# Optimization experiments

Measured on AMD Instinct MI355X. Metric: run time of the kernel, lower is better.

## Reference

```python
import jax, jax.numpy as jnp
import numpy as np

B, T, N = 512, 200, 256
ENC_G, ENC_C = 256, 256
C_DIM, G_DIM, U_DIM, F_DIM = 128, 256, 64, 64
CLIP = 5.0


def _gru(x, h, Wih, Whh, bih, bhh):
    # PyTorch nn.GRUCell math
    gi = x @ Wih.T + bih
    gh = h @ Whh.T + bhh
    ir, iz, inn = jnp.split(gi, 3, axis=-1)
    hr, hz, hn = jnp.split(gh, 3, axis=-1)
    r = jax.nn.sigmoid(ir + hr)
    z = jax.nn.sigmoid(iz + hz)
    n = jnp.tanh(inn + r * hn)
    return (1.0 - z) * n + z * h


def setup_inputs() -> dict:
    key = jax.random.key(0)
    ks = iter(jax.random.split(key, 64))

    def gru_p(i, h):
        return (jax.random.normal(next(ks), (3 * h, i)) * i ** -0.5,
                jax.random.normal(next(ks), (3 * h, h)) * h ** -0.5,
                jnp.zeros(3 * h), jnp.zeros(3 * h))

    def lin_p(i, o):
        return (jax.random.normal(next(ks), (o, i)) * i ** -0.5, jnp.zeros(o))

    inp = {}
    inp['x'] = jax.random.uniform(next(ks), (B, T, N))
    inp['eps_g0'] = jax.random.normal(next(ks), (B, G_DIM))
    inp['eps_u'] = jax.random.normal(next(ks), (B, T, U_DIM))
    for name, (i, h) in [('gf', (N, ENC_G)), ('gb', (N, ENC_G)),
                         ('cf', (N, ENC_C)), ('cb', (N, ENC_C)),
                         ('ct', (2 * ENC_C + F_DIM, C_DIM)), ('gn', (U_DIM, G_DIM))]:
        Wih, Whh, bih, bhh = gru_p(i, h)
        inp['Wih_' + name] = Wih; inp['Whh_' + name] = Whh
        inp['bih_' + name] = bih; inp['bhh_' + name] = bhh
    for name, (i, o) in [('g0m', (2 * ENC_G, G_DIM)), ('g0v', (2 * ENC_G, G_DIM)),
                         ('um', (C_DIM, U_DIM)), ('uv', (C_DIM, U_DIM)),
                         ('f', (G_DIM, F_DIM)), ('r', (F_DIM, N))]:
        W, b = lin_p(i, o)
        inp['W_' + name] = W; inp['b_' + name] = b
    return inp


def reference(x, eps_g0, eps_u,
              Wih_gf, Whh_gf, bih_gf, bhh_gf,
              Wih_gb, Whh_gb, bih_gb, bhh_gb,
              Wih_cf, Whh_cf, bih_cf, bhh_cf,
              Wih_cb, Whh_cb, bih_cb, bhh_cb,
              Wih_ct, Whh_ct, bih_ct, bhh_ct,
              Wih_gn, Whh_gn, bih_gn, bhh_gn,
              W_g0m, b_g0m, W_g0v, b_g0v,
              W_um, b_um, W_uv, b_uv,
              W_f, b_f, W_r, b_r):
    Bsz = x.shape[0]
    xs = x.transpose(1, 0, 2)  # [T, B, N]
    zg = jnp.zeros((Bsz, ENC_G), x.dtype)
    zc = jnp.zeros((Bsz, ENC_C), x.dtype)

    def make_enc(pg, pc):
        def step(carry, xt):
            hg, hc = carry
            hg = jnp.minimum(_gru(xt, hg, *pg), CLIP)   # clamp(max=clip_val)
            hc = jnp.minimum(_gru(xt, hc, *pc), CLIP)
            return (hg, hc), hc
        return step

    (hgf, _), hcf = jax.lax.scan(
        make_enc((Wih_gf, Whh_gf, bih_gf, bhh_gf), (Wih_cf, Whh_cf, bih_cf, bhh_cf)),
        (zg, zc), xs)
    (hgb, _), hcb = jax.lax.scan(
        make_enc((Wih_gb, Whh_gb, bih_gb, bhh_gb), (Wih_cb, Whh_cb, bih_cb, bhh_cb)),
        (zg, zc), xs[::-1])
    h_enc_g = jnp.concatenate([hgf, hgb], axis=-1)        # [B, 2*ENC_G]
    h_enc_c = jnp.concatenate([hcf, hcb[::-1]], axis=-1)  # [T, B, 2*ENC_C]

    g0_mean = h_enc_g @ W_g0m.T + b_g0m
    g0_logv = jnp.log(jnp.exp(h_enc_g @ W_g0v.T + b_g0v) + 1e-4)
    g0 = eps_g0 * jnp.exp(0.5 * g0_logv) + g0_mean

    f0 = g0 @ W_f.T + b_f
    hc0 = jnp.zeros((Bsz, C_DIM), x.dtype)

    def gen_step(carry, inp):
        h_c, g, f = carry
        henc_t, eps_t = inp
        cin = jnp.concatenate([henc_t, f], axis=-1)
        h_c = jnp.clip(_gru(cin, h_c, Wih_ct, Whh_ct, bih_ct, bhh_ct), 0.0, CLIP)
        um = h_c @ W_um.T + b_um
        ul = h_c @ W_uv.T + b_uv
        u = eps_t * jnp.exp(0.5 * ul) + um
        g = jnp.clip(_gru(u, g, Wih_gn, Whh_gn, bih_gn, bhh_gn), 0.0, CLIP)
        f = g @ W_f.T + b_f
        return (h_c, g, f), (um, ul, f)

    _, (u_means, u_logvs, factors) = jax.lax.scan(
        gen_step, (hc0, g0, f0), (h_enc_c, eps_u.transpose(1, 0, 2)))
    factors = factors.transpose(1, 0, 2)  # [B, T, F_DIM]
    rates = jnp.exp(jnp.clip(factors @ W_r.T + b_r, -CLIP, CLIP))
    return (g0_mean, g0_logv,
            u_means.transpose(1, 0, 2), u_logvs.transpose(1, 0, 2),
            factors, rates)
```

## Files before the change

kernel.cpp:

```cpp
#include <hip/hip_runtime.h>
#include <hip/hip_bf16.h>
#include <stdint.h>

typedef __bf16 bf16x8 __attribute__((ext_vector_type(8)));
typedef __bf16 bf16x4 __attribute__((ext_vector_type(4)));
typedef float  f32x4  __attribute__((ext_vector_type(4)));
typedef unsigned short u16x8 __attribute__((ext_vector_type(8)));

#define MFMA_B16(A_,B_,C_) __builtin_amdgcn_mfma_f32_16x16x32_bf16((A_),(B_),(C_),0,0,0)

static constexpr int TT = 200;
static constexpr int TC = 25;
static constexpr int NCH = 8;

static __device__ __forceinline__ float sig_f(float x){ return 1.f/(1.f+__expf(-x)); }
static __device__ __forceinline__ float tanh_f(float x){
  float e = __expf(-2.f*fabsf(x));
  float t = (1.f-e)/(1.f+e);
  return x<0.f ? -t : t;
}
static __device__ __forceinline__ float bf2f(unsigned short u){
  union{unsigned int i; float f;} v; v.i = ((unsigned)u)<<16; return v.f;
}
static __device__ __forceinline__ void pin8(bf16x8 &v){ asm volatile("" : "+v"(v)); }

static __device__ __forceinline__ int swz_off(int row, int col_bytes, int strideB){
  return (row*strideB + col_bytes) ^ ((row&7)<<4);
}
static __device__ __forceinline__ bf16x8 lds_rdA(const __bf16* buf, int row, int kt, int lq, int strideB){
  return *(const bf16x8*)((const char*)buf + swz_off(row, kt*64 + lq*16, strideB));
}
static __device__ __forceinline__ void lds_wr(__bf16* buf, int row, int dim, int strideB, float v){
  *(__bf16*)((char*)buf + swz_off(row, dim*2, strideB)) = (__bf16)v;
}
static __device__ __forceinline__ void lds_barrier(){
  asm volatile("s_waitcnt lgkmcnt(0)" ::: "memory");
  __builtin_amdgcn_s_barrier();
}

__global__ void cvt_bf16(const float* __restrict__ s, __bf16* __restrict__ d, int n){
  int i = blockIdx.x*blockDim.x + threadIdx.x;
  int st = gridDim.x*blockDim.x;
  for(; i<n; i+=st) d[i] = (__bf16)s[i];
}

__global__ __launch_bounds__(256) void gi_gemm(const float* __restrict__ x,
                                               const __bf16* __restrict__ Wall,
                                               __bf16* __restrict__ gi, int t0){
  const int tid=threadIdx.x, w=tid>>6, l=tid&63, lr=l&15, lq=l>>4;
  const int cell = blockIdx.y;
  const bool fwd = (cell&1)==0;
  const int m0 = blockIdx.x*64;
  const int tloc = m0>>9, b0 = m0&511;
  const int tabs = fwd ? (t0+tloc) : (TT-1-(t0+tloc));
  const int brow = b0 + w*16 + lr;

  const float* xp = x + (size_t)brow*TT*256 + (size_t)tabs*256 + lq*8;
  bf16x8 a[8];
  #pragma unroll
  for(int kt=0;kt<8;kt++){
    float4 f0 = *(const float4*)(xp + kt*32);
    float4 f1 = *(const float4*)(xp + kt*32 + 4);
    bf16x8 v;
    v[0]=(__bf16)f0.x; v[1]=(__bf16)f0.y; v[2]=(__bf16)f0.z; v[3]=(__bf16)f0.w;
    v[4]=(__bf16)f1.x; v[5]=(__bf16)f1.y; v[6]=(__bf16)f1.z; v[7]=(__bf16)f1.w;
    a[kt]=v;
  }
  const __bf16* Wc = Wall + (size_t)cell*768*256;
  #pragma unroll 1
  for(int nt=0;nt<48;nt++){
    f32x4 acc={};
    const __bf16* bp = Wc + (size_t)(nt*16+lr)*256 + lq*8;
    #pragma unroll
    for(int kt=0;kt<8;kt++)
      acc = MFMA_B16(a[kt], *(const bf16x8*)(bp + kt*32), acc);
    bf16x4 pk;
    pk[0]=(__bf16)acc[0]; pk[1]=(__bf16)acc[1]; pk[2]=(__bf16)acc[2]; pk[3]=(__bf16)acc[3];
    *(bf16x4*)(gi + (((size_t)cell*TC + tloc)*768 + nt*16+lr)*512 + b0 + w*16 + lq*4) = pk;
  }
}

struct EncP{
  const __bf16* whh;
  const float*  bih[4];
  const float*  bhh[4];
  const __bf16* gi;
  __bf16* henc;
  float*  hcar;
  int t0;
};
__global__ __launch_bounds__(512,2) void enc_scan(EncP P){
  const int tid=threadIdx.x, w=tid>>6, l=tid&63, lr=l&15, lq=l>>4;
  const int cell=blockIdx.y, b0=blockIdx.x*16;
  const bool fwd = (cell&1)==0;
  const bool isC = cell>=2;
  const int dim0 = w*32;

  __shared__ __align__(16) __bf16 hA[2][16*256];
  __shared__ __align__(16) __bf16 giL[2][768*16];
  __shared__ float blds[1024];

  for(int d=tid; d<256; d+=512){
    blds[d]     = P.bih[cell][d]     + P.bhh[cell][d];
    blds[256+d] = P.bih[cell][256+d] + P.bhh[cell][256+d];
    blds[512+d] = P.bih[cell][512+d];
    blds[768+d] = P.bhh[cell][512+d];
  }
  const __bf16* Wh = P.whh + (size_t)cell*768*256;
  bf16x8 wreg[2][2][8];
  #pragma unroll
  for(int jt=0;jt<2;jt++)
    #pragma unroll
    for(int g=0;g<2;g++)
      #pragma unroll
      for(int kt=0;kt<8;kt++){
        wreg[jt][g][kt] = *(const bf16x8*)(Wh + (size_t)(g*256 + dim0 + jt*16 + lr)*256 + kt*32 + lq*8);
        pin8(wreg[jt][g][kt]);
      }
  f32x4 hold[2];
  #pragma unroll
  for(int jt=0;jt<2;jt++)
    #pragma unroll
    for(int rr=0;rr<4;rr++){
      float v = P.hcar[((size_t)cell*512 + b0 + lq*4+rr)*256 + dim0 + jt*16 + lr];
      hold[jt][rr] = v;
      lds_wr(hA[0], lq*4+rr, dim0+jt*16+lr, 512, v);
    }
  const int prow = w*96 + (l>>1), phal = l&1;
  const __bf16* gbase = P.gi + ((size_t)cell*TC*768 + prow)*512 + b0 + phal*8;
  u16x8 pf0, pf1, pf2;
  pf0 = *(const u16x8*)(gbase + (size_t)0*768*512 +  0*512);
  pf1 = *(const u16x8*)(gbase + (size_t)0*768*512 + 32*512);
  pf2 = *(const u16x8*)(gbase + (size_t)0*768*512 + 64*512);
  __syncthreads();
  {
    __bf16* gl = giL[0] + prow*16 + phal*8;
    *(u16x8*)(gl)        = pf0;
    *(u16x8*)(gl+32*16)  = pf1;
    *(u16x8*)(gl+64*16)  = pf2;
  }
  { int sn = 1 < TC ? 1 : TC-1;
    pf0 = *(const u16x8*)(gbase + (size_t)sn*768*512 +  0*512);
    pf1 = *(const u16x8*)(gbase + (size_t)sn*768*512 + 32*512);
    pf2 = *(const u16x8*)(gbase + (size_t)sn*768*512 + 64*512);
  }
  lds_barrier();

  int p=0, q=0;
  #pragma unroll 1
  for(int s=0;s<TC;s++){
    const int tglob = P.t0 + s;
    const int tx = fwd ? tglob : (TT-1-tglob);
    if(s+1<TC){
      __bf16* gl = giL[1-q] + prow*16 + phal*8;
      *(u16x8*)(gl)        = pf0;
      *(u16x8*)(gl+32*16)  = pf1;
      *(u16x8*)(gl+64*16)  = pf2;
    }
    { int sn = (s+2<TC) ? s+2 : TC-1;
      pf0 = *(const u16x8*)(gbase + (size_t)sn*768*512 +  0*512);
      pf1 = *(const u16x8*)(gbase + (size_t)sn*768*512 + 32*512);
      pf2 = *(const u16x8*)(gbase + (size_t)sn*768*512 + 64*512);
    }
    const __bf16* gq = giL[q];
    #pragma unroll
    for(int jt=0;jt<2;jt++){
      const int d = dim0 + jt*16 + lr;
      const __bf16* whN = Wh + (size_t)(512 + d)*256 + lq*8;
      f32x4 aR={}, aZ={}, aH={};
      #pragma unroll
      for(int kt=0;kt<8;kt++){
        bf16x8 frag = lds_rdA(hA[p], lr, kt, lq, 512);
        aR = MFMA_B16(frag, wreg[jt][0][kt], aR);
        aZ = MFMA_B16(frag, wreg[jt][1][kt], aZ);
        aH = MFMA_B16(frag, *(const bf16x8*)(whN + kt*32), aH);
      }
      ushort4 gR = *(const ushort4*)(gq + (0*256+d)*16 + lq*4);
      ushort4 gZ = *(const ushort4*)(gq + (1*256+d)*16 + lq*4);
      ushort4 gN = *(const ushort4*)(gq + (2*256+d)*16 + lq*4);
      const float bR=blds[d], bZ=blds[256+d], bI=blds[512+d], bH=blds[768+d];
      const unsigned short* uR=(const unsigned short*)&gR;
      const unsigned short* uZ=(const unsigned short*)&gZ;
      const unsigned short* uN=(const unsigned short*)&gN;
      #pragma unroll
      for(int rr=0;rr<4;rr++){
        float r = sig_f(aR[rr] + bf2f(uR[rr]) + bR);
        float z = sig_f(aZ[rr] + bf2f(uZ[rr]) + bZ);
        float nn= tanh_f(bf2f(uN[rr]) + bI + r*(aH[rr] + bH));
        float h = (1.f-z)*nn + z*hold[jt][rr];
        h = fminf(h, 5.f);
        hold[jt][rr] = h;
        lds_wr(hA[1-p], lq*4+rr, d, 512, h);
      }
    }
    if(isC){
      const int row = l>>2, dgrp = (l&3)*8;
      bf16x8 hv = *(const bf16x8*)((const char*)hA[1-p] +
                    ((row*512 + (dim0+dgrp)*2) ^ ((row&7)<<4)));
      *(bf16x8*)(P.henc + ((size_t)tx*512 + b0 + row)*512 + (cell==3?256:0) + dim0 + dgrp) = hv;
    }
    lds_barrier();
    p ^= 1; q ^= 1;
  }
  #pragma unroll
  for(int jt=0;jt<2;jt++)
    #pragma unroll
    for(int rr=0;rr<4;rr++)
      P.hcar[((size_t)cell*512 + b0 + lq*4+rr)*256 + dim0 + jt*16 + lr] = hold[jt][rr];
}

__global__ void g0_kernel(const float* __restrict__ hgf, const float* __restrict__ hgb,
                          const float* __restrict__ Wm, const float* __restrict__ bm,
                          const float* __restrict__ Wv, const float* __restrict__ bv,
                          const float* __restrict__ eps,
                          float* __restrict__ o_mean, float* __restrict__ o_logv,
                          float* __restrict__ g0){
  int j = blockIdx.x*blockDim.x + threadIdx.x;
  int b = j>>8, d = j&255;
  const float4* hf=(const float4*)(hgf + (size_t)b*256);
  const float4* hb=(const float4*)(hgb + (size_t)b*256);
  const float4* mp=(const float4*)(Wm + (size_t)d*512);
  const float4* vp=(const float4*)(Wv + (size_t)d*512);
  float am=0.f, av=0.f;
  #pragma unroll 4
  for(int k=0;k<64;k++){
    float4 h=hf[k], m=mp[k], v=vp[k];
    am += h.x*m.x + h.y*m.y + h.z*m.z + h.w*m.w;
    av += h.x*v.x + h.y*v.y + h.z*v.z + h.w*v.w;
  }
  #pragma unroll 4
  for(int k=0;k<64;k++){
    float4 h=hb[k], m=mp[64+k], v=vp[64+k];
    am += h.x*m.x + h.y*m.y + h.z*m.z + h.w*m.w;
    av += h.x*v.x + h.y*v.y + h.z*v.z + h.w*v.w;
  }
  float mean = am + bm[d];
  float ev   = __expf(av + bv[d]) + 1e-4f;
  float lv   = __logf(ev);
  o_mean[j]=mean; o_logv[j]=lv;
  g0[j] = eps[j]*sqrtf(ev) + mean;
}

__global__ __launch_bounds__(256,2) void gict_gemm(const __bf16* __restrict__ henc,
                                                   const __bf16* __restrict__ wct,
                                                   __bf16* __restrict__ gictT){
  const int tid=threadIdx.x, w=tid>>6, l=tid&63, lr=l&15, lq=l>>4;
  const int m0 = blockIdx.x*8 + w*2;
  bf16x8 a[2][16];
  #pragma unroll
  for(int m=0;m<2;m++){
    const __bf16* ap = henc + (size_t)((m0+m)*16 + lr)*512 + lq*8;
    #pragma unroll
    for(int kt=0;kt<16;kt++) a[m][kt] = *(const bf16x8*)(ap + kt*32);
  }
  #pragma unroll 1
  for(int nt=0;nt<24;nt++){
    f32x4 c0={}, c1={};
    const __bf16* bp = wct + (size_t)(nt*16+lr)*576 + lq*8;
    #pragma unroll
    for(int kt=0;kt<16;kt++){
      bf16x8 bb = *(const bf16x8*)(bp + kt*32);
      c0 = MFMA_B16(a[0][kt], bb, c0);
      c1 = MFMA_B16(a[1][kt], bb, c1);
    }
    #pragma unroll
    for(int m=0;m<2;m++){
      f32x4 c = m? c1 : c0;
      int R0 = (m0+m)*16 + lq*4;
      int t  = R0>>9, b = R0&511;
      bf16x4 pk;
      pk[0]=(__bf16)c[0]; pk[1]=(__bf16)c[1]; pk[2]=(__bf16)c[2]; pk[3]=(__bf16)c[3];
      *(bf16x4*)(gictT + ((size_t)t*384 + nt*16+lr)*512 + b) = pk;
    }
  }
}

struct GenP{
  const __bf16 *wct, *whh_ct, *wih_gn, *whh_gn, *w_um, *w_uv, *w_f;
  const float  *bih_ct, *bhh_ct, *bih_gn, *bhh_gn, *b_um, *b_uv, *b_f;
  const __bf16* gihT;
  const float*  g0;
  const float*  eps_u;
  float *o_um, *o_ul, *o_f;
};
__global__ __launch_bounds__(512,2) void gen_scan(GenP P){
  const int tid=threadIdx.x, w=tid>>6, l=tid&63, lr=l&15, lq=l>>4;
  const int b0 = blockIdx.x*16;

  __shared__ __align__(16) __bf16 wgnL[768*64];
  __shared__ __align__(16) __bf16 hcA[2][16*128];
  __shared__ __align__(16) __bf16 gA [2][16*256];
  __shared__ __align__(16) __bf16 uA [16*64];
  __shared__ __align__(16) __bf16 fA [16*64];

  for(int c=tid; c<6144; c+=512){
    int row = c>>3, part = c&7;
    bf16x8 v = *(const bf16x8*)(P.wih_gn + (size_t)row*64 + part*8);
    *(bf16x8*)((char*)wgnL + ((row*128 + part*16) ^ ((row&7)<<4))) = v;
  }
  bf16x8 wrz[2][2][8];
  #pragma unroll
  for(int jt=0;jt<2;jt++)
    #pragma unroll
    for(int g=0;g<2;g++)
      #pragma unroll
      for(int kt=0;kt<8;kt++){
        wrz[jt][g][kt] = *(const bf16x8*)(P.whh_gn + (size_t)(g*256 + w*32 + jt*16 + lr)*256 + kt*32 + lq*8);
        pin8(wrz[jt][g][kt]);
      }

  const int dct = w*16 + lr;
  const int duu = (w&3)*16 + lr;
  const int duf = (w&3)*16 + lr;
  const float bctR = P.bih_ct[dct]     + P.bhh_ct[dct];
  const float bctZ = P.bih_ct[128+dct] + P.bhh_ct[128+dct];
  const float bctI = P.bih_ct[256+dct];
  const float bctH = P.bhh_ct[256+dct];
  float bgnR[2], bgnZ[2], bgnI[2], bgnH[2];
  #pragma unroll
  for(int jt=0;jt<2;jt++){
    int d = w*32 + jt*16 + lr;
    bgnR[jt] = P.bih_gn[d]     + P.bhh_gn[d];
    bgnZ[jt] = P.bih_gn[256+d] + P.bhh_gn[256+d];
    bgnI[jt] = P.bih_gn[512+d];
    bgnH[jt] = P.bhh_gn[512+d];
  }
  const float bum = P.b_um[duu], buv = P.b_uv[duu], bff = P.b_f[duf];

  f32x4 gC[2], hcC;
  hcC = (f32x4){};
  #pragma unroll
  for(int jt=0;jt<2;jt++)
    #pragma unroll
    for(int rr=0;rr<4;rr++){
      float v = P.g0[(size_t)(b0+lq*4+rr)*256 + w*32 + jt*16 + lr];
      gC[jt][rr] = v;
      lds_wr(gA[0], lq*4+rr, w*32+jt*16+lr, 512, v);
    }
  for(int i=tid;i<16*128;i+=512) hcA[0][i] = (__bf16)0.f;
  __syncthreads();
  if(w>=4){
    f32x4 fa={};
    #pragma unroll
    for(int kt=0;kt<8;kt++){
      bf16x8 gf = lds_rdA(gA[0], lr, kt, lq, 512);
      fa = MFMA_B16(gf, *(const bf16x8*)(P.w_f + (size_t)duf*256 + kt*32 + lq*8), fa);
    }
    #pragma unroll
    for(int rr=0;rr<4;rr++) lds_wr(fA, lq*4+rr, duf, 128, fa[rr]+bff);
  }
  ushort4 gpR, gpZ, gpN; float epf[4];
  gpR = *(const ushort4*)(P.gihT + ((size_t)0*384 +       dct)*512 + b0 + lq*4);
  gpZ = *(const ushort4*)(P.gihT + ((size_t)0*384 + 128 + dct)*512 + b0 + lq*4);
  gpN = *(const ushort4*)(P.gihT + ((size_t)0*384 + 256 + dct)*512 + b0 + lq*4);
  if(w<4){
    #pragma unroll
    for(int rr=0;rr<4;rr++) epf[rr] = P.eps_u[((size_t)(b0+lq*4+rr)*TT + 0)*64 + duu];
  }
  bf16x8 cwh[3][4];
  #pragma unroll
  for(int g=0;g<3;g++)
    #pragma unroll
    for(int kt=0;kt<4;kt++)
      cwh[g][kt] = *(const bf16x8*)(P.whh_ct + (size_t)(g*128+dct)*128 + kt*32 + lq*8);
  __syncthreads();

  int pc=0, pg=0;
  #pragma unroll 1
  for(int t=0;t<TT;t++){
    {
      bf16x8 ff0 = lds_rdA(fA, lr, 0, lq, 128);
      bf16x8 ff1 = lds_rdA(fA, lr, 1, lq, 128);
      bf16x8 hp0 = lds_rdA(hcA[pc], lr, 0, lq, 256);
      bf16x8 hp1 = lds_rdA(hcA[pc], lr, 1, lq, 256);
      bf16x8 hp2 = lds_rdA(hcA[pc], lr, 2, lq, 256);
      bf16x8 hp3 = lds_rdA(hcA[pc], lr, 3, lq, 256);
      f32x4 aR={}, aZ={}, aI={}, aH={};
      #pragma unroll
      for(int g=0;g<3;g++){
        const __bf16* wif = P.wct + (size_t)(g*128+dct)*576 + 512 + lq*8;
        bf16x8 wf0 = *(const bf16x8*)(wif);
        bf16x8 wf1 = *(const bf16x8*)(wif + 32);
        if(g==0){
          aR = MFMA_B16(ff0,wf0,aR); aR = MFMA_B16(ff1,wf1,aR);
          aR = MFMA_B16(hp0,cwh[0][0],aR); aR = MFMA_B16(hp1,cwh[0][1],aR);
          aR = MFMA_B16(hp2,cwh[0][2],aR); aR = MFMA_B16(hp3,cwh[0][3],aR);
        }else if(g==1){
          aZ = MFMA_B16(ff0,wf0,aZ); aZ = MFMA_B16(ff1,wf1,aZ);
          aZ = MFMA_B16(hp0,cwh[1][0],aZ); aZ = MFMA_B16(hp1,cwh[1][1],aZ);
          aZ = MFMA_B16(hp2,cwh[1][2],aZ); aZ = MFMA_B16(hp3,cwh[1][3],aZ);
        }else{
          aI = MFMA_B16(ff0,wf0,aI); aI = MFMA_B16(ff1,wf1,aI);
          aH = MFMA_B16(hp0,cwh[2][0],aH); aH = MFMA_B16(hp1,cwh[2][1],aH);
          aH = MFMA_B16(hp2,cwh[2][2],aH); aH = MFMA_B16(hp3,cwh[2][3],aH);
        }
      }
      const unsigned short* uR=(const unsigned short*)&gpR;
      const unsigned short* uZ=(const unsigned short*)&gpZ;
      const unsigned short* uN=(const unsigned short*)&gpN;
      #pragma unroll
      for(int rr=0;rr<4;rr++){
        float r = sig_f(aR[rr] + bf2f(uR[rr]) + bctR);
        float z = sig_f(aZ[rr] + bf2f(uZ[rr]) + bctZ);
        float nn= tanh_f(aI[rr] + bf2f(uN[rr]) + bctI + r*(aH[rr] + bctH));
        float h = (1.f-z)*nn + z*hcC[rr];
        h = fminf(fmaxf(h,0.f), 5.f);
        hcC[rr] = h;
        lds_wr(hcA[1-pc], lq*4+rr, dct, 256, h);
      }
    }
    lds_barrier();

    if(w<4){
      bf16x8 hn0 = lds_rdA(hcA[1-pc], lr, 0, lq, 256);
      bf16x8 hn1 = lds_rdA(hcA[1-pc], lr, 1, lq, 256);
      bf16x8 hn2 = lds_rdA(hcA[1-pc], lr, 2, lq, 256);
      bf16x8 hn3 = lds_rdA(hcA[1-pc], lr, 3, lq, 256);
      f32x4 am={}, av={};
      const __bf16* wm = P.w_um + (size_t)duu*128 + lq*8;
      const __bf16* wv = P.w_uv + (size_t)duu*128 + lq*8;
      am = MFMA_B16(hn0, *(const bf16x8*)(wm   ), am);
      am = MFMA_B16(hn1, *(const bf16x8*)(wm+32), am);
      am = MFMA_B16(hn2, *(const bf16x8*)(wm+64), am);
      am = MFMA_B16(hn3, *(const bf16x8*)(wm+96), am);
      av = MFMA_B16(hn0, *(const bf16x8*)(wv   ), av);
      av = MFMA_B16(hn1, *(const bf16x8*)(wv+32), av);
      av = MFMA_B16(hn2, *(const bf16x8*)(wv+64), av);
      av = MFMA_B16(hn3, *(const bf16x8*)(wv+96), av);
      #pragma unroll
      for(int rr=0;rr<4;rr++){
        const int row = lq*4+rr;
        float um = am[rr] + bum;
        float ul = av[rr] + buv;
        size_t oi = ((size_t)(b0+row)*TT + t)*64 + duu;
        P.o_um[oi] = um;
        P.o_ul[oi] = ul;
        float u = epf[rr]*__expf(0.5f*ul) + um;
        lds_wr(uA, row, duu, 128, u);
      }
    }
    bf16x8 wn0[8];
    #pragma unroll
    for(int kt=0;kt<8;kt++)
      wn0[kt] = *(const bf16x8*)(P.whh_gn + (size_t)(512 + w*32 + lr)*256 + kt*32 + lq*8);
    lds_barrier();

    {
      const int tn = (t+1<TT)? t+1 : TT-1;
      gpR = *(const ushort4*)(P.gihT + ((size_t)tn*384 +       dct)*512 + b0 + lq*4);
      gpZ = *(const ushort4*)(P.gihT + ((size_t)tn*384 + 128 + dct)*512 + b0 + lq*4);
      gpN = *(const ushort4*)(P.gihT + ((size_t)tn*384 + 256 + dct)*512 + b0 + lq*4);
      if(w<4){
        #pragma unroll
        for(int rr=0;rr<4;rr++) epf[rr] = P.eps_u[((size_t)(b0+lq*4+rr)*TT + tn)*64 + duu];
      }
      bf16x8 uf0 = lds_rdA(uA, lr, 0, lq, 128);
      bf16x8 uf1 = lds_rdA(uA, lr, 1, lq, 128);
      #pragma unroll
      for(int jt=0;jt<2;jt++){
        const int dg = w*32 + jt*16 + lr;
        bf16x8 wn[8];
        if(jt==0){
          #pragma unroll
          for(int kt=0;kt<8;kt++) wn[kt] = wn0[kt];
        }else{
          #pragma unroll
          for(int kt=0;kt<8;kt++)
            wn[kt] = *(const bf16x8*)(P.whh_gn + (size_t)(512 + dg)*256 + kt*32 + lq*8);
        }
        f32x4 aR={}, aZ={}, aI={}, aH={};
        #pragma unroll
        for(int g=0;g<3;g++){
          const int row = g*256 + dg;
          bf16x8 w0 = *(const bf16x8*)((const char*)wgnL + ((row*128 +  0 + lq*16) ^ ((row&7)<<4)));
          bf16x8 w1 = *(const bf16x8*)((const char*)wgnL + ((row*128 + 64 + lq*16) ^ ((row&7)<<4)));
          if(g==0){ aR = MFMA_B16(uf0,w0,aR); aR = MFMA_B16(uf1,w1,aR); }
          else if(g==1){ aZ = MFMA_B16(uf0,w0,aZ); aZ = MFMA_B16(uf1,w1,aZ); }
          else { aI = MFMA_B16(uf0,w0,aI); aI = MFMA_B16(uf1,w1,aI); }
        }
        #pragma unroll
        for(int kt=0;kt<8;kt++){
          bf16x8 gf = lds_rdA(gA[pg], lr, kt, lq, 512);
          aR = MFMA_B16(gf, wrz[jt][0][kt], aR);
          aZ = MFMA_B16(gf, wrz[jt][1][kt], aZ);
          aH = MFMA_B16(gf, wn[kt], aH);
        }
        #pragma unroll
        for(int rr=0;rr<4;rr++){
          float r = sig_f(aR[rr] + bgnR[jt]);
          float z = sig_f(aZ[rr] + bgnZ[jt]);
          float nn= tanh_f(aI[rr] + bgnI[jt] + r*(aH[rr] + bgnH[jt]));
          float gv = (1.f-z)*nn + z*gC[jt][rr];
          gv = fminf(fmaxf(gv,0.f), 5.f);
          gC[jt][rr] = gv;
          lds_wr(gA[1-pg], lq*4+rr, dg, 512, gv);
        }
      }
    }
    lds_barrier();

    if(w>=4){
      f32x4 fa={};
      const __bf16* wfp = P.w_f + (size_t)duf*256 + lq*8;
      #pragma unroll
      for(int kt=0;kt<8;kt++){
        bf16x8 gf = lds_rdA(gA[1-pg], lr, kt, lq, 512);
        fa = MFMA_B16(gf, *(const bf16x8*)(wfp + kt*32), fa);
      }
      #pragma unroll
      for(int rr=0;rr<4;rr++){
        const int row = lq*4+rr;
        float v = fa[rr] + bff;
        P.o_f[((size_t)(b0+row)*TT + t)*64 + duf] = v;
        lds_wr(fA, row, duf, 128, v);
      }
    }
    #pragma unroll
    for(int g=0;g<3;g++)
      #pragma unroll
      for(int kt=0;kt<4;kt++)
        cwh[g][kt] = *(const bf16x8*)(P.whh_ct + (size_t)(g*128+dct)*128 + kt*32 + lq*8);
    lds_barrier();
    pc ^= 1; pg ^= 1;
  }
}

__global__ void rates_k(const float* __restrict__ fac, const float* __restrict__ Wr,
                        const float* __restrict__ br, float* __restrict__ out){
  const int total = 512*200*256;
  int i = blockIdx.x*blockDim.x + threadIdx.x;
  int st = gridDim.x*blockDim.x;
  for(; i<total; i+=st){
    int row = i>>8, n = i&255;
    const float4* fp=(const float4*)(fac + (size_t)row*64);
    const float4* wp=(const float4*)(Wr  + (size_t)n*64);
    float a = 0.f;
    #pragma unroll
    for(int k=0;k<16;k++){
      float4 f=fp[k], ww=wp[k];
      a += f.x*ww.x + f.y*ww.y + f.z*ww.z + f.w*ww.w;
    }
    a += br[n];
    a = fminf(fmaxf(a, -5.f), 5.f);
    out[i] = __expf(a);
  }
}

extern "C" void kernel_launch(void* const* d_in, const int* in_sizes, int n_in,
                              void* d_out, int out_size, void* d_ws, size_t ws_size,
                              hipStream_t stream){
  (void)in_sizes; (void)n_in; (void)out_size; (void)ws_size;
  const float* x      = (const float*)d_in[0];
  const float* eps_g0 = (const float*)d_in[1];
  const float* eps_u  = (const float*)d_in[2];
  const float* Wih_f[6]; const float* Whh_f[6]; const float* bih[6]; const float* bhh[6];
  for(int c=0;c<6;c++){
    Wih_f[c]=(const float*)d_in[3+4*c]; Whh_f[c]=(const float*)d_in[4+4*c];
    bih[c]  =(const float*)d_in[5+4*c]; bhh[c]  =(const float*)d_in[6+4*c];
  }
  const float* W_g0m=(const float*)d_in[27]; const float* b_g0m=(const float*)d_in[28];
  const float* W_g0v=(const float*)d_in[29]; const float* b_g0v=(const float*)d_in[30];
  const float* W_um =(const float*)d_in[31]; const float* b_um =(const float*)d_in[32];
  const float* W_uv =(const float*)d_in[33]; const float* b_uv =(const float*)d_in[34];
  const float* W_f  =(const float*)d_in[35]; const float* b_f  =(const float*)d_in[36];
  const float* W_r  =(const float*)d_in[37]; const float* b_r  =(const float*)d_in[38];

  char* ws = (char*)d_ws; size_t off = 0;
  auto alloc = [&](size_t bytes)->char*{
    char* p = ws + off; off = (off + bytes + 255) & ~(size_t)255; return p;
  };
  __bf16* wencall = (__bf16*)alloc((size_t)4*768*256*2);
  __bf16* whhall  = (__bf16*)alloc((size_t)4*768*256*2);
  __bf16* wct_b   = (__bf16*)alloc((size_t)384*576*2);
  __bf16* whhct_b = (__bf16*)alloc((size_t)384*128*2);
  __bf16* wihgn_b = (__bf16*)alloc((size_t)768*64*2);
  __bf16* whhgn_b = (__bf16*)alloc((size_t)768*256*2);
  __bf16* wum_b   = (__bf16*)alloc((size_t)64*128*2);
  __bf16* wuv_b   = (__bf16*)alloc((size_t)64*128*2);
  __bf16* wf_b    = (__bf16*)alloc((size_t)64*256*2);
  __bf16* henc    = (__bf16*)alloc((size_t)200*512*512*2);
  __bf16* gi_buf  = (__bf16*)alloc((size_t)4*TC*768*512*2);
  float*  hcar    = (float*)alloc((size_t)4*512*256*4);
  float*  g0buf   = (float*)alloc((size_t)512*256*4);

  for(int c=0;c<4;c++){
    cvt_bf16<<<128,256,0,stream>>>(Wih_f[c], wencall + (size_t)c*768*256, 768*256);
    cvt_bf16<<<128,256,0,stream>>>(Whh_f[c], whhall  + (size_t)c*768*256, 768*256);
  }
  cvt_bf16<<<128,256,0,stream>>>(Wih_f[4], wct_b,   384*576);
  cvt_bf16<<<64 ,256,0,stream>>>(Whh_f[4], whhct_b, 384*128);
  cvt_bf16<<<64 ,256,0,stream>>>(Wih_f[5], wihgn_b, 768*64);
  cvt_bf16<<<128,256,0,stream>>>(Whh_f[5], whhgn_b, 768*256);
  cvt_bf16<<<32 ,256,0,stream>>>(W_um, wum_b, 64*128);
  cvt_bf16<<<32 ,256,0,stream>>>(W_uv, wuv_b, 64*128);
  cvt_bf16<<<32 ,256,0,stream>>>(W_f,  wf_b,  64*256);
  hipMemsetAsync(hcar, 0, (size_t)4*512*256*4, stream);

  EncP ep;
  ep.whh = whhall;
  for(int c=0;c<4;c++){ ep.bih[c]=bih[c]; ep.bhh[c]=bhh[c]; }
  ep.gi = gi_buf; ep.henc = henc; ep.hcar = hcar;
  for(int k=0;k<NCH;k++){
    gi_gemm<<<dim3((512*TC)/64,4),256,0,stream>>>(x, wencall, gi_buf, k*TC);
    ep.t0 = k*TC;
    enc_scan<<<dim3(32,4),512,0,stream>>>(ep);
  }

  float* out = (float*)d_out;
  float* o_mean = out;
  float* o_logv = out + 131072;
  float* o_um   = out + 262144;
  float* o_ul   = out + 6815744;
  float* o_f    = out + 13369344;
  float* o_r    = out + 19922944;

  g0_kernel<<<512,256,0,stream>>>(hcar + 0, hcar + (size_t)1*512*256,
                                  W_g0m,b_g0m, W_g0v,b_g0v, eps_g0,
                                  o_mean,o_logv, g0buf);
  gict_gemm<<<800,256,0,stream>>>(henc, wct_b, gi_buf);

  GenP gp;
  gp.wct=wct_b; gp.whh_ct=whhct_b; gp.wih_gn=wihgn_b; gp.whh_gn=whhgn_b;
  gp.w_um=wum_b; gp.w_uv=wuv_b; gp.w_f=wf_b;
  gp.bih_ct=bih[4]; gp.bhh_ct=bhh[4]; gp.bih_gn=bih[5]; gp.bhh_gn=bhh[5];
  gp.b_um=b_um; gp.b_uv=b_uv; gp.b_f=b_f;
  gp.gihT=gi_buf; gp.g0=g0buf; gp.eps_u=eps_u;
  gp.o_um=o_um; gp.o_ul=o_ul; gp.o_f=o_f;
  gen_scan<<<32,512,0,stream>>>(gp);

  rates_k<<<8192,256,0,stream>>>(o_f, W_r, b_r, o_r);
}
```

Before: 7.520 ms.

## Keep recurrent weights in registers and pre-transpose eps for gen scan

Relaxes launch bounds of enc_scan and gen_scan to one block per SM so the n-gate recurrent weights and the f-part of W_ct can live in registers. Per-step global weight loads for W_um/W_uv, W_hh_gn n-gate and W_f are hoisted or issued earlier to overlap with other work. A new kernel transposes eps_u to time-major layout (reusing the henc buffer after gict_gemm) so per-step eps loads are contiguous. This trades register pressure and occupancy for fewer latency-bound loads on the serial scan path.

Measured after the change: 8.461 ms. 12.5% more time.

```diff
diff --git a/kernel.cpp b/kernel.cpp
--- a/kernel.cpp
+++ b/kernel.cpp
@@ -42,6 +42,17 @@
   int i = blockIdx.x*blockDim.x + threadIdx.x;
   int st = gridDim.x*blockDim.x;
   for(; i<n; i+=st) d[i] = (__bf16)s[i];
+}
+
+__global__ void epsT_k(const float4* __restrict__ e, float4* __restrict__ o){
+  const int total = 512*200*16;
+  int j = blockIdx.x*blockDim.x + threadIdx.x;
+  int st = gridDim.x*blockDim.x;
+  for(; j<total; j+=st){
+    int b = j/3200, rem = j - b*3200;
+    int t = rem>>4, dq = rem&15;
+    o[((size_t)t*512 + b)*16 + dq] = e[j];
+  }
 }
 
 __global__ __launch_bounds__(256) void gi_gemm(const float* __restrict__ x,
@@ -89,7 +100,7 @@
   float*  hcar;
   int t0;
 };
-__global__ __launch_bounds__(512,2) void enc_scan(EncP P){
+__global__ __launch_bounds__(512,1) void enc_scan(EncP P){
   const int tid=threadIdx.x, w=tid>>6, l=tid&63, lr=l&15, lq=l>>4;
   const int cell=blockIdx.y, b0=blockIdx.x*16;
   const bool fwd = (cell&1)==0;
@@ -107,11 +118,11 @@
     blds[768+d] = P.bhh[cell][512+d];
   }
   const __bf16* Wh = P.whh + (size_t)cell*768*256;
-  bf16x8 wreg[2][2][8];
+  bf16x8 wreg[2][3][8];
   #pragma unroll
   for(int jt=0;jt<2;jt++)
     #pragma unroll
-    for(int g=0;g<2;g++)
+    for(int g=0;g<3;g++)
       #pragma unroll
       for(int kt=0;kt<8;kt++){
         wreg[jt][g][kt] = *(const bf16x8*)(Wh + (size_t)(g*256 + dim0 + jt*16 + lr)*256 + kt*32 + lq*8);
@@ -166,14 +177,13 @@
     #pragma unroll
     for(int jt=0;jt<2;jt++){
       const int d = dim0 + jt*16 + lr;
-      const __bf16* whN = Wh + (size_t)(512 + d)*256 + lq*8;
       f32x4 aR={}, aZ={}, aH={};
       #pragma unroll
       for(int kt=0;kt<8;kt++){
         bf16x8 frag = lds_rdA(hA[p], lr, kt, lq, 512);
         aR = MFMA_B16(frag, wreg[jt][0][kt], aR);
         aZ = MFMA_B16(frag, wreg[jt][1][kt], aZ);
-        aH = MFMA_B16(frag, *(const bf16x8*)(whN + kt*32), aH);
+        aH = MFMA_B16(frag, wreg[jt][2][kt], aH);
       }
       ushort4 gR = *(const ushort4*)(gq + (0*256+d)*16 + lq*4);
       ushort4 gZ = *(const ushort4*)(gq + (1*256+d)*16 + lq*4);
@@ -280,10 +290,10 @@
   const float  *bih_ct, *bhh_ct, *bih_gn, *bhh_gn, *b_um, *b_uv, *b_f;
   const __bf16* gihT;
   const float*  g0;
-  const float*  eps_u;
+  const float*  epsT;
   float *o_um, *o_ul, *o_f;
 };
-__global__ __launch_bounds__(512,2) void gen_scan(GenP P){
+__global__ __launch_bounds__(512,1) void gen_scan(GenP P){
   const int tid=threadIdx.x, w=tid>>6, l=tid&63, lr=l&15, lq=l>>4;
   const int b0 = blockIdx.x*16;
 
@@ -311,7 +321,6 @@
 
   const int dct = w*16 + lr;
   const int duu = (w&3)*16 + lr;
-  const int duf = (w&3)*16 + lr;
   const float bctR = P.bih_ct[dct]     + P.bhh_ct[dct];
   const float bctZ = P.bih_ct[128+dct] + P.bhh_ct[128+dct];
   const float bctI = P.bih_ct[256+dct];
@@ -325,7 +334,7 @@
     bgnI[jt] = P.bih_gn[512+d];
     bgnH[jt] = P.bhh_gn[512+d];
   }
-  const float bum = P.b_um[duu], buv = P.b_uv[duu], bff = P.b_f[duf];
+  const float bum = P.b_um[duu], buv = P.b_uv[duu], bff = P.b_f[duu];
 
   f32x4 gC[2], hcC;
   hcC = (f32x4){};
@@ -344,10 +353,10 @@
     #pragma unroll
     for(int kt=0;kt<8;kt++){
       bf16x8 gf = lds_rdA(gA[0], lr, kt, lq, 512);
-      fa = MFMA_B16(gf, *(const bf16x8*)(P.w_f + (size_t)duf*256 + kt*32 + lq*8), fa);
-    }
-    #pragma unroll
-    for(int rr=0;rr<4;rr++) lds_wr(fA, lq*4+rr, duf, 128, fa[rr]+bff);
+      fa = MFMA_B16(gf, *(const bf16x8*)(P.w_f + (size_t)duu*256 + kt*32 + lq*8), fa);
+    }
+    #pragma unroll
+    for(int rr=0;rr<4;rr++) lds_wr(fA, lq*4+rr, duu, 128, fa[rr]+bff);
   }
   ushort4 gpR, gpZ, gpN; float epf[4];
   gpR = *(const ushort4*)(P.gihT + ((size_t)0*384 +       dct)*512 + b0 + lq*4);
@@ -355,19 +364,32 @@
   gpN = *(const ushort4*)(P.gihT + ((size_t)0*384 + 256 + dct)*512 + b0 + lq*4);
   if(w<4){
     #pragma unroll
-    for(int rr=0;rr<4;rr++) epf[rr] = P.eps_u[((size_t)(b0+lq*4+rr)*TT + 0)*64 + duu];
-  }
-  bf16x8 cwh[3][4];
-  #pragma unroll
-  for(int g=0;g<3;g++)
+    for(int rr=0;rr<4;rr++) epf[rr] = P.epsT[((size_t)0*512 + b0+lq*4+rr)*64 + duu];
+  }
+  bf16x8 cwh[3][4], wctf[3][2];
+  #pragma unroll
+  for(int g=0;g<3;g++){
     #pragma unroll
     for(int kt=0;kt<4;kt++)
       cwh[g][kt] = *(const bf16x8*)(P.whh_ct + (size_t)(g*128+dct)*128 + kt*32 + lq*8);
+    wctf[g][0] = *(const bf16x8*)(P.wct + (size_t)(g*128+dct)*576 + 512 + lq*8);
+    wctf[g][1] = *(const bf16x8*)(P.wct + (size_t)(g*128+dct)*576 + 512 + 32 + lq*8);
+  }
   __syncthreads();
 
   int pc=0, pg=0;
   #pragma unroll 1
   for(int t=0;t<TT;t++){
+    bf16x8 wmv[8];
+    if(w<4){
+      const __bf16* wm = P.w_um + (size_t)duu*128 + lq*8;
+      const __bf16* wv = P.w_uv + (size_t)duu*128 + lq*8;
+      #pragma unroll
+      for(int kt=0;kt<4;kt++){
+        wmv[kt]   = *(const bf16x8*)(wm + kt*32);
+        wmv[4+kt] = *(const bf16x8*)(wv + kt*32);
+      }
+    }
     {
       bf16x8 ff0 = lds_rdA(fA, lr, 0, lq, 128);
       bf16x8 ff1 = lds_rdA(fA, lr, 1, lq, 128);
@@ -376,25 +398,15 @@
       bf16x8 hp2 = lds_rdA(hcA[pc], lr, 2, lq, 256);
       bf16x8 hp3 = lds_rdA(hcA[pc], lr, 3, lq, 256);
       f32x4 aR={}, aZ={}, aI={}, aH={};
-      #pragma unroll
-      for(int g=0;g<3;g++){
-        const __bf16* wif = P.wct + (size_t)(g*128+dct)*576 + 512 + lq*8;
-        bf16x8 wf0 = *(const bf16x8*)(wif);
-        bf16x8 wf1 = *(const bf16x8*)(wif + 32);
-        if(g==0){
-          aR = MFMA_B16(ff0,wf0,aR); aR = MFMA_B16(ff1,wf1,aR);
-          aR = MFMA_B16(hp0,cwh[0][0],aR); aR = MFMA_B16(hp1,cwh[0][1],aR);
-          aR = MFMA_B16(hp2,cwh[0][2],aR); aR = MFMA_B16(hp3,cwh[0][3],aR);
-        }else if(g==1){
-          aZ = MFMA_B16(ff0,wf0,aZ); aZ = MFMA_B16(ff1,wf1,aZ);
-          aZ = MFMA_B16(hp0,cwh[1][0],aZ); aZ = MFMA_B16(hp1,cwh[1][1],aZ);
-          aZ = MFMA_B16(hp2,cwh[1][2],aZ); aZ = MFMA_B16(hp3,cwh[1][3],aZ);
-        }else{
-          aI = MFMA_B16(ff0,wf0,aI); aI = MFMA_B16(ff1,wf1,aI);
-          aH = MFMA_B16(hp0,cwh[2][0],aH); aH = MFMA_B16(hp1,cwh[2][1],aH);
-          aH = MFMA_B16(hp2,cwh[2][2],aH); aH = MFMA_B16(hp3,cwh[2][3],aH);
-        }
-      }
+      aR = MFMA_B16(ff0,wctf[0][0],aR); aR = MFMA_B16(ff1,wctf[0][1],aR);
+      aR = MFMA_B16(hp0,cwh[0][0],aR);  aR = MFMA_B16(hp1,cwh[0][1],aR);
+      aR = MFMA_B16(hp2,cwh[0][2],aR);  aR = MFMA_B16(hp3,cwh[0][3],aR);
+      aZ = MFMA_B16(ff0,wctf[1][0],aZ); aZ = MFMA_B16(ff1,wctf[1][1],aZ);
+      aZ = MFMA_B16(hp0,cwh[1][0],aZ);  aZ = MFMA_B16(hp1,cwh[1][1],aZ);
+      aZ = MFMA_B16(hp2,cwh[1][2],aZ);  aZ = MFMA_B16(hp3,cwh[1][3],aZ);
+      aI = MFMA_B16(ff0,wctf[2][0],aI); aI = MFMA_B16(ff1,wctf[2][1],aI);
+      aH = MFMA_B16(hp0,cwh[2][0],aH);  aH = MFMA_B16(hp1,cwh[2][1],aH);
+      aH = MFMA_B16(hp2,cwh[2][2],aH);  aH = MFMA_B16(hp3,cwh[2][3],aH);
       const unsigned short* uR=(const unsigned short*)&gpR;
       const unsigned short* uZ=(const unsigned short*)&gpZ;
       const unsigned short* uN=(const unsigned short*)&gpN;
@@ -411,22 +423,26 @@
     }
     lds_barrier();
 
+    bf16x8 wnh[2][8];
+    #pragma unroll
+    for(int jt=0;jt<2;jt++)
+      #pragma unroll
+      for(int kt=0;kt<8;kt++)
+        wnh[jt][kt] = *(const bf16x8*)(P.whh_gn + (size_t)(512 + w*32 + jt*16 + lr)*256 + kt*32 + lq*8);
     if(w<4){
       bf16x8 hn0 = lds_rdA(hcA[1-pc], lr, 0, lq, 256);
       bf16x8 hn1 = lds_rdA(hcA[1-pc], lr, 1, lq, 256);
       bf16x8 hn2 = lds_rdA(hcA[1-pc], lr, 2, lq, 256);
       bf16x8 hn3 = lds_rdA(hcA[1-pc], lr, 3, lq, 256);
       f32x4 am={}, av={};
-      const __bf16* wm = P.w_um + (size_t)duu*128 + lq*8;
-      const __bf16* wv = P.w_uv + (size_t)duu*128 + lq*8;
-      am = MFMA_B16(hn0, *(const bf16x8*)(wm   ), am);
-      am = MFMA_B16(hn1, *(const bf16x8*)(wm+32), am);
-      am = MFMA_B16(hn2, *(const bf16x8*)(wm+64), am);
-      am = MFMA_B16(hn3, *(const bf16x8*)(wm+96), am);
-      av = MFMA_B16(hn0, *(const bf16x8*)(wv   ), av);
-      av = MFMA_B16(hn1, *(const bf16x8*)(wv+32), av);
-      av = MFMA_B16(hn2, *(const bf16x8*)(wv+64), av);
-      av = MFMA_B16(hn3, *(const bf16x8*)(wv+96), av);
+      am = MFMA_B16(hn0, wmv[0], am);
+      am = MFMA_B16(hn1, wmv[1], am);
+      am = MFMA_B16(hn2, wmv[2], am);
+      am = MFMA_B16(hn3, wmv[3], am);
+      av = MFMA_B16(hn0, wmv[4], av);
+      av = MFMA_B16(hn1, wmv[5], av);
+      av = MFMA_B16(hn2, wmv[6], av);
+      av = MFMA_B16(hn3, wmv[7], av);
       #pragma unroll
       for(int rr=0;rr<4;rr++){
         const int row = lq*4+rr;
@@ -439,12 +455,9 @@
         lds_wr(uA, row, duu, 128, u);
       }
     }
-    bf16x8 wn0[8];
-    #pragma unroll
-    for(int kt=0;kt<8;kt++)
-      wn0[kt] = *(const bf16x8*)(P.whh_gn + (size_t)(512 + w*32 + lr)*256 + kt*32 + lq*8);
     lds_barrier();
 
+    bf16x8 wfh[8];
     {
       const int tn = (t+1<TT)? t+1 : TT-1;
       gpR = *(const ushort4*)(P.gihT + ((size_t)tn*384 +       dct)*512 + b0 + lq*4);
@@ -452,22 +465,13 @@
       gpN = *(const ushort4*)(P.gihT + ((size_t)tn*384 + 256 + dct)*512 + b0 + lq*4);
       if(w<4){
         #pragma unroll
-        for(int rr=0;rr<4;rr++) epf[rr] = P.eps_u[((size_t)(b0+lq*4+rr)*TT + tn)*64 + duu];
+        for(int rr=0;rr<4;rr++) epf[rr] = P.epsT[((size_t)tn*512 + b0+lq*4+rr)*64 + duu];
       }
       bf16x8 uf0 = lds_rdA(uA, lr, 0, lq, 128);
       bf16x8 uf1 = lds_rdA(uA, lr, 1, lq, 128);
       #pragma unroll
       for(int jt=0;jt<2;jt++){
         const int dg = w*32 + jt*16 + lr;
-        bf16x8 wn[8];
-        if(jt==0){
-          #pragma unroll
-          for(int kt=0;kt<8;kt++) wn[kt] = wn0[kt];
-        }else{
-          #pragma unroll
-          for(int kt=0;kt<8;kt++)
-            wn[kt] = *(const bf16x8*)(P.whh_gn + (size_t)(512 + dg)*256 + kt*32 + lq*8);
-        }
         f32x4 aR={}, aZ={}, aI={}, aH={};
         #pragma unroll
         for(int g=0;g<3;g++){
@@ -483,7 +487,12 @@
           bf16x8 gf = lds_rdA(gA[pg], lr, kt, lq, 512);
           aR = MFMA_B16(gf, wrz[jt][0][kt], aR);
           aZ = MFMA_B16(gf, wrz[jt][1][kt], aZ);
-          aH = MFMA_B16(gf, wn[kt], aH);
+          aH = MFMA_B16(gf, wnh[jt][kt], aH);
+        }
+        if(jt==0 && w>=4){
+          const __bf16* wfp = P.w_f + (size_t)duu*256 + lq*8;
+          #pragma unroll
+          for(int kt=0;kt<8;kt++) wfh[kt] = *(const bf16x8*)(wfp + kt*32);
         }
         #pragma unroll
         for(int rr=0;rr<4;rr++){
@@ -501,25 +510,27 @@
 
     if(w>=4){
       f32x4 fa={};
-      const __bf16* wfp = P.w_f + (size_t)duf*256 + lq*8;
       #pragma unroll
       for(int kt=0;kt<8;kt++){
         bf16x8 gf = lds_rdA(gA[1-pg], lr, kt, lq, 512);
-        fa = MFMA_B16(gf, *(const bf16x8*)(wfp + kt*32), fa);
+        fa = MFMA_B16(gf, wfh[kt], fa);
       }
       #pragma unroll
       for(int rr=0;rr<4;rr++){
         const int row = lq*4+rr;
         float v = fa[rr] + bff;
-        P.o_f[((size_t)(b0+row)*TT + t)*64 + duf] = v;
-        lds_wr(fA, row, duf, 128, v);
-      }
-    }
-    #pragma unroll
-    for(int g=0;g<3;g++)
+        P.o_f[((size_t)(b0+row)*TT + t)*64 + duu] = v;
+        lds_wr(fA, row, duu, 128, v);
+      }
+    }
+    #pragma unroll
+    for(int g=0;g<3;g++){
       #pragma unroll
       for(int kt=0;kt<4;kt++)
         cwh[g][kt] = *(const bf16x8*)(P.whh_ct + (size_t)(g*128+dct)*128 + kt*32 + lq*8);
+      wctf[g][0] = *(const bf16x8*)(P.wct + (size_t)(g*128+dct)*576 + 512 + lq*8);
+      wctf[g][1] = *(const bf16x8*)(P.wct + (size_t)(g*128+dct)*576 + 512 + 32 + lq*8);
+    }
     lds_barrier();
     pc ^= 1; pg ^= 1;
   }
@@ -619,12 +630,15 @@
                                   o_mean,o_logv, g0buf);
   gict_gemm<<<800,256,0,stream>>>(henc, wct_b, gi_buf);
 
+  float* epsT = (float*)henc;
+  epsT_k<<<2048,256,0,stream>>>((const float4*)eps_u, (float4*)epsT);
+
   GenP gp;
   gp.wct=wct_b; gp.whh_ct=whhct_b; gp.wih_gn=wihgn_b; gp.whh_gn=whhgn_b;
   gp.w_um=wum_b; gp.w_uv=wuv_b; gp.w_f=wf_b;
   gp.bih_ct=bih[4]; gp.bhh_ct=bhh[4]; gp.bih_gn=bih[5]; gp.bhh_gn=bhh[5];
   gp.b_um=b_um; gp.b_uv=b_uv; gp.b_f=b_f;
-  gp.gihT=gi_buf; gp.g0=g0buf; gp.eps_u=eps_u;
+  gp.gihT=gi_buf; gp.g0=g0buf; gp.epsT=epsT;
   gp.o_um=o_um; gp.o_ul=o_ul; gp.o_f=o_f;
   gen_scan<<<32,512,0,stream>>>(gp);
 
```
